# Kernel tuning notes

Measured on AMD Instinct MI355X. Metric: run time of the kernel, lower is better.

## Reference

```python
import jax, jax.numpy as jnp
import numpy as np

B, S, D, H, NS = 4, 2048, 1024, 16, 300
DK = D // H                      # 64
NSP = (NS + H - 1) // H * H      # 304 (padded skills)
DG = NSP // H                    # 19
NEG_FILL = -1e9                  # fp32 path in the torch module


def setup_inputs() -> dict:
    key = jax.random.key(0)
    ks = jax.random.split(key, 12)
    sc = 0.02
    return {
        "context_sequence": jax.random.normal(ks[0], (B, S, D), jnp.float32),
        "value_sequence": jax.random.normal(ks[1], (B, S, NS), jnp.float32),
        "mask": jnp.triu(jnp.ones((S, S), jnp.bool_), k=1),  # causal: True = masked
        # weights stored as [in, out] (math-equivalent to torch's x @ W.T + b)
        "Wq": jax.random.normal(ks[2], (D, D), jnp.float32) * sc,
        "bq": jnp.zeros((D,), jnp.float32),
        "Wk": jax.random.normal(ks[3], (D, D), jnp.float32) * sc,
        "bk": jnp.zeros((D,), jnp.float32),
        "Wv": jax.random.normal(ks[4], (NS, NS), jnp.float32) * sc,
        "bv": jnp.zeros((NS,), jnp.float32),
        "Wg": jax.random.normal(ks[5], (NS, D), jnp.float32) * sc,  # gain_to_context
        "bg": jnp.zeros((D,), jnp.float32),
        "Wo": jax.random.normal(ks[6], (D, D), jnp.float32) * sc,   # output_proj
        "bo": jnp.zeros((D,), jnp.float32),
    }


def reference(context_sequence, value_sequence, mask,
              Wq, bq, Wk, bk, Wv, bv, Wg, bg, Wo, bo):
    b = context_sequence.shape[0]
    orig_dtype = context_sequence.dtype

    # Q, K: [b, H, S, DK]
    Q = (context_sequence @ Wq + bq).reshape(b, -1, H, DK).transpose(0, 2, 1, 3)
    K = (context_sequence @ Wk + bk).reshape(b, -1, H, DK).transpose(0, 2, 1, 3)

    # intrinsic-gain V: project in skill space, zero-pad to NSP, split heads -> [b, H, S, DG]
    V_proj = value_sequence @ Wv + bv
    V_proj = jnp.pad(V_proj, ((0, 0), (0, 0), (0, NSP - NS)))
    V = V_proj.reshape(b, -1, H, DG).transpose(0, 2, 1, 3)

    # fp32 score upcast, scale by sqrt(d_k), mask, cast back, softmax
    scores = jnp.einsum('bhqd,bhkd->bhqk',
                        Q.astype(jnp.float32), K.astype(jnp.float32)) / np.sqrt(DK)
    scores = jnp.where(mask, NEG_FILL, scores).astype(orig_dtype)
    attn = jax.nn.softmax(scores, axis=-1)

    # [b, H, S, DG] -> [b, S, NSP] -> slice to NS
    head_gains = jnp.einsum('bhqk,bhkd->bhqd', attn, V)
    agg = head_gains.transpose(0, 2, 1, 3).reshape(b, -1, NSP)[..., :NS]

    output = agg @ Wg + bg            # gain_to_context
    return output @ Wo + bo           # output_proj (dropout is identity in eval)
```

## Files before the change

### kernel.cpp

```cpp
#include <hip/hip_runtime.h>
#include <hip/hip_bf16.h>

#define MROWS 8192
#define DMODEL 1024
#define SLEN 2048
#define NHEADS 16
#define DKH 64
#define DGH 19
#define NSKILL 300
#define KGPAD 320
#define AGG_LD 320
#define QK_LD 2048
#define VK 320
#define VTN 384

typedef __attribute__((ext_vector_type(8))) short short8;
typedef __attribute__((ext_vector_type(4))) float floatx4;

__device__ __forceinline__ float bf2f(unsigned short u) {
  union { unsigned int i; float f; } cv;
  cv.i = ((unsigned int)u) << 16;
  return cv.f;
}
__device__ __forceinline__ unsigned short f2bf(float f) {
  __hip_bfloat16 h = __float2bfloat16(f);
  unsigned short u;
  __builtin_memcpy(&u, &h, 2);
  return u;
}

__device__ __forceinline__ void ld8(const float* p, float* v) {
  float4 a = *(const float4*)p;
  float4 b = *((const float4*)p + 1);
  v[0]=a.x; v[1]=a.y; v[2]=a.z; v[3]=a.w;
  v[4]=b.x; v[5]=b.y; v[6]=b.z; v[7]=b.w;
}
__device__ __forceinline__ void st1(float* p, float v) { *p = v; }
__device__ __forceinline__ void st1(__hip_bfloat16* p, float v) {
  unsigned short raw = f2bf(v); __builtin_memcpy(p, &raw, 2);
}
__device__ __forceinline__ void st8(__hip_bfloat16* p, const float* v) {
  ushort4 a, b;
  a.x=f2bf(v[0]); a.y=f2bf(v[1]); a.z=f2bf(v[2]); a.w=f2bf(v[3]);
  b.x=f2bf(v[4]); b.y=f2bf(v[5]); b.z=f2bf(v[6]); b.w=f2bf(v[7]);
  *(ushort4*)p = a;
  *((ushort4*)p + 1) = b;
}

__device__ __forceinline__ void gl_lds16(const void* g, void* l) {
  __builtin_amdgcn_global_load_lds(
      (const __attribute__((address_space(1))) unsigned int*)g,
      (__attribute__((address_space(3))) unsigned int*)l, 16, 0, 0);
}

__global__ __launch_bounds__(256)
void convert_bf16_kernel(const float* __restrict__ in,
                         __hip_bfloat16* __restrict__ out, int nelem)
{
  int i = (blockIdx.x * 256 + threadIdx.x) * 4;
  if (i < nelem) {
    float4 v = *(const float4*)(in + i);
    ushort4 s;
    s.x = f2bf(v.x); s.y = f2bf(v.y); s.z = f2bf(v.z); s.w = f2bf(v.w);
    *(ushort4*)((__hip_bfloat16*)out + i) = s;
  }
}

__global__ __launch_bounds__(256)
void convert_v_kernel(const float* __restrict__ in,
                      __hip_bfloat16* __restrict__ out)
{
  int idx = blockIdx.x * 256 + threadIdx.x;
  int row = idx / 40;
  int c8  = (idx - row * 40) * 8;
  const float* ip = in + (size_t)row * NSKILL + c8;
  float v[8];
  if (c8 + 8 <= NSKILL) {
    ld8(ip, v);
  } else {
    #pragma unroll
    for (int u = 0; u < 8; u++)
      v[u] = (c8 + u < NSKILL) ? ip[u] : 0.f;
  }
  st8(out + (size_t)row * VK + c8, v);
}

__global__ __launch_bounds__(256)
void convert_wg_kernel(const float* __restrict__ Wg,
                       __hip_bfloat16* __restrict__ Wgb)
{
  int i4 = (blockIdx.x * 256 + threadIdx.x) * 4;
  int r = i4 >> 10;
  ushort4 s = {0, 0, 0, 0};
  if (r < NSKILL) {
    float4 v = *(const float4*)(Wg + i4);
    s.x = f2bf(v.x); s.y = f2bf(v.y); s.z = f2bf(v.z); s.w = f2bf(v.w);
  }
  *(ushort4*)((__hip_bfloat16*)Wgb + i4) = s;
}

__global__ __launch_bounds__(256)
void build_biases_kernel(const float* __restrict__ bq, const float* __restrict__ bk,
                         const float* __restrict__ bv,
                         float* __restrict__ biasqk, float* __restrict__ biasv,
                         float* __restrict__ z384)
{
  int t = threadIdx.x;
  for (int i = t; i < 1024; i += 256) { biasqk[i] = bq[i]; biasqk[1024 + i] = bk[i]; }
  for (int i = t; i < 384; i += 256) {
    biasv[i] = (i < NSKILL) ? bv[i] : 0.f;
    z384[i] = 0.f;
  }
}

__global__ __launch_bounds__(256)
void bgo_kernel(const float* __restrict__ bg, const float* __restrict__ Wo,
                const float* __restrict__ bo, float* __restrict__ bgo)
{
  __shared__ float red[256];
  const int c   = threadIdx.x & 15;
  const int jg  = threadIdx.x >> 4;
  const int col = blockIdx.x * 16 + c;
  float acc = 0.f;
  const int j0 = jg * 64;
  #pragma unroll 8
  for (int j = j0; j < j0 + 64; j++)
    acc = fmaf(bg[j], Wo[(size_t)j * DMODEL + col], acc);
  red[threadIdx.x] = acc;
  __syncthreads();
  if (jg == 0) {
    float s = 0.f;
    #pragma unroll
    for (int g = 0; g < 16; g++) s += red[g*16 + c];
    bgo[col] = s + bo[col];
  }
}

__global__ __launch_bounds__(256)
void transpose_w_kernel(const float* __restrict__ W,
                        __hip_bfloat16* __restrict__ Wt,
                        int K, int Nld, int Ntrue, int Kpad)
{
  __shared__ float t[32][33];
  const int k0 = blockIdx.x * 32;
  const int n0 = blockIdx.y * 32;
  const int tx = threadIdx.x & 31, ty = threadIdx.x >> 5;
  #pragma unroll
  for (int i = 0; i < 4; i++) {
    int k = k0 + ty + i*8;
    int nn = n0 + tx;
    t[ty + i*8][tx] = (k < K && nn < Ntrue) ? W[(size_t)k * Nld + nn] : 0.f;
  }
  __syncthreads();
  #pragma unroll
  for (int i = 0; i < 4; i++) {
    int nn = n0 + ty + i*8;
    int kk = k0 + tx;
    st1(Wt + (size_t)nn * Kpad + kk, t[tx][ty + i*8]);
  }
}

template<typename TC>
__global__ __launch_bounds__(256)
void gemm_mfma_bt(const __hip_bfloat16* __restrict__ A,
                  const __hip_bfloat16* __restrict__ Bt,
                  const float* __restrict__ bias,
                  TC* __restrict__ C, int ldc,
                  int M, int N, int K, int lda, int ldb)
{
  __shared__ __align__(16) short Al[128*64];
  __shared__ __align__(16) short Bl[128*64];
  const int tid  = threadIdx.x;
  const int lane = tid & 63;
  const int wave = tid >> 6;
  const int wy = wave >> 1;
  const int wx = wave & 1;
  const int n    = lane & 15;
  const int quad = lane >> 4;

  const int m0 = blockIdx.y * 128;
  const int n0 = blockIdx.x * 128;

  floatx4 acc[4][4];
  #pragma unroll
  for (int i = 0; i < 4; i++)
    #pragma unroll
    for (int j = 0; j < 4; j++) acc[i][j] = (floatx4){0.f,0.f,0.f,0.f};

  const short* Ag = (const short*)A;
  const short* Bg = (const short*)Bt;

  for (int k0 = 0; k0 < K; k0 += 64) {
    #pragma unroll
    for (int it = 0; it < 4; it++) {
      int ci = it*256 + tid;
      int r = ci >> 3, c = ci & 7;
      int cs = c ^ (r & 7);
      gl_lds16(Ag + (size_t)(m0 + r) * lda + k0 + cs*8, &Al[ci*8]);
    }
    #pragma unroll
    for (int it = 0; it < 4; it++) {
      int ci = it*256 + tid;
      int r = ci >> 3, c = ci & 7;
      int cs = c ^ (r & 7);
      gl_lds16(Bg + (size_t)(n0 + r) * ldb + k0 + cs*8, &Bl[ci*8]);
    }
    __syncthreads();

    #pragma unroll
    for (int s = 0; s < 2; s++) {
      short8 af[4], bfr[4];
      const int c = s*4 + quad;
      #pragma unroll
      for (int i = 0; i < 4; i++) {
        int r = wy*64 + i*16 + n;
        af[i] = *(const short8*)&Al[(r*8 + (c ^ (r & 7)))*8];
      }
      #pragma unroll
      for (int j = 0; j < 4; j++) {
        int r = wx*64 + j*16 + n;
        bfr[j] = *(const short8*)&Bl[(r*8 + (c ^ (r & 7)))*8];
      }
      #pragma unroll
      for (int i = 0; i < 4; i++)
        #pragma unroll
        for (int j = 0; j < 4; j++)
          acc[i][j] = __builtin_amdgcn_mfma_f32_16x16x32_bf16(af[i], bfr[j], acc[i][j], 0, 0, 0);
    }
    __syncthreads();
  }

  float bj[4];
  #pragma unroll
  for (int j = 0; j < 4; j++) bj[j] = bias[n0 + wx*64 + j*16 + n];
  #pragma unroll
  for (int i = 0; i < 4; i++) {
    #pragma unroll
    for (int r = 0; r < 4; r++) {
      int row = m0 + wy*64 + i*16 + quad*4 + r;
      TC* cp = C + (size_t)row * ldc;
      #pragma unroll
      for (int j = 0; j < 4; j++) {
        int col = n0 + wx*64 + j*16 + n;
        st1(cp + col, acc[i][j][r] + bj[j]);
      }
    }
  }
}

__global__ __launch_bounds__(256)
void gemm_mfma_bt_tv(const __hip_bfloat16* __restrict__ A,
                     const __hip_bfloat16* __restrict__ Bt,
                     const float* __restrict__ bias,
                     __hip_bfloat16* __restrict__ VT,
                     int M, int N, int K, int lda, int ldb)
{
  __shared__ __align__(16) short Al[128*64];
  __shared__ __align__(16) short Bl[128*64];
  const int tid  = threadIdx.x;
  const int lane = tid & 63;
  const int wave = tid >> 6;
  const int wy = wave >> 1;
  const int wx = wave & 1;
  const int n    = lane & 15;
  const int quad = lane >> 4;

  const int m0 = blockIdx.y * 128;
  const int n0 = blockIdx.x * 128;

  floatx4 acc[4][4];
  #pragma unroll
  for (int i = 0; i < 4; i++)
    #pragma unroll
    for (int j = 0; j < 4; j++) acc[i][j] = (floatx4){0.f,0.f,0.f,0.f};

  const short* Ag = (const short*)A;
  const short* Bg = (const short*)Bt;

  for (int k0 = 0; k0 < K; k0 += 64) {
    #pragma unroll
    for (int it = 0; it < 4; it++) {
      int ci = it*256 + tid;
      int r = ci >> 3, c = ci & 7;
      int cs = c ^ (r & 7);
      gl_lds16(Ag + (size_t)(m0 + r) * lda + k0 + cs*8, &Al[ci*8]);
    }
    #pragma unroll
    for (int it = 0; it < 4; it++) {
      int ci = it*256 + tid;
      int r = ci >> 3, c = ci & 7;
      int cs = c ^ (r & 7);
      gl_lds16(Bg + (size_t)(n0 + r) * ldb + k0 + cs*8, &Bl[ci*8]);
    }
    __syncthreads();

    #pragma unroll
    for (int s = 0; s < 2; s++) {
      short8 af[4], bfr[4];
      const int c = s*4 + quad;
      #pragma unroll
      for (int i = 0; i < 4; i++) {
        int r = wy*64 + i*16 + n;
        af[i] = *(const short8*)&Al[(r*8 + (c ^ (r & 7)))*8];
      }
      #pragma unroll
      for (int j = 0; j < 4; j++) {
        int r = wx*64 + j*16 + n;
        bfr[j] = *(const short8*)&Bl[(r*8 + (c ^ (r & 7)))*8];
      }
      #pragma unroll
      for (int i = 0; i < 4; i++)
        #pragma unroll
        for (int j = 0; j < 4; j++)
          acc[i][j] = __builtin_amdgcn_mfma_f32_16x16x32_bf16(af[i], bfr[j], acc[i][j], 0, 0, 0);
    }
    __syncthreads();
  }

  float bj[4];
  #pragma unroll
  for (int j = 0; j < 4; j++) bj[j] = bias[n0 + wx*64 + j*16 + n];
  #pragma unroll
  for (int i = 0; i < 4; i++) {
    int row0 = m0 + wy*64 + i*16 + quad*4;
    int bb = row0 >> 11, rin = row0 & 2047;
    #pragma unroll
    for (int j = 0; j < 4; j++) {
      int col = n0 + wx*64 + j*16 + n;
      ushort4 pk;
      pk.x = f2bf(acc[i][j][0] + bj[j]);
      pk.y = f2bf(acc[i][j][1] + bj[j]);
      pk.z = f2bf(acc[i][j][2] + bj[j]);
      pk.w = f2bf(acc[i][j][3] + bj[j]);
      *(ushort4*)(VT + ((size_t)bb * VTN + col) * SLEN + rin) = pk;
    }
  }
}

#define ATT_BM 128
#define ATT_BK 64
#define ATT_GRID 1024

__global__ __launch_bounds__(256)
void attn_mfma_kernel(const __hip_bfloat16* __restrict__ Qb,
                      const __hip_bfloat16* __restrict__ Kb,
                      const __hip_bfloat16* __restrict__ VTg,
                      __hip_bfloat16* __restrict__ Agg)
{
  __shared__ __align__(16) short Kf[64*64];
  __shared__ __align__(16) short Vf[32*64];
  __shared__ __align__(16) unsigned int Pl[4][2][2][4][16][4];

  const int tid  = threadIdx.x;
  const int lane = tid & 63;
  const int wave = tid >> 6;
  const int n    = lane & 15;
  const int quad = lane >> 4;

  const int raw = blockIdx.x;
  const int grp = raw >> 6;
  const int qt  = (grp < 8) ? (15 - grp) : (grp - 8);
  const int bh  = raw & 63;
  const int h   = bh & 15;
  const int b   = bh >> 4;
  const int qbase = qt * ATT_BM;
  const size_t bS = (size_t)b * SLEN;

  short8 qf[2][2];
  #pragma unroll
  for (int rf = 0; rf < 2; rf++)
    #pragma unroll
    for (int ks = 0; ks < 2; ks++) {
      const __hip_bfloat16* qp = Qb + (bS + qbase + wave*32 + rf*16 + n) * QK_LD
                                    + h*DKH + ks*32 + quad*8;
      short8 v = *(const short8*)qp;
      #pragma unroll
      for (int e = 0; e < 8; e++) {
        float f = bf2f((unsigned short)v[e]) * 0.125f;
        v[e] = (short)f2bf(f);
      }
      qf[rf][ks] = v;
    }

  const short* kp;
  {
    int f = tid;
    int nn = f & 15, q = (f >> 4) & 3, c = (f >> 6) & 3;
    kp = (const short*)Kb + (bS + c*16 + nn) * QK_LD + h*DKH + q*8;
  }
  const short* vp;
  {
    int g = tid;
    int vn = g & 15, vq = (g >> 4) & 3, sv = (g >> 6) & 1, cv = g >> 7;
    vp = (const short*)VTg + ((size_t)b * VTN + h*DGH + cv*16 + vn) * SLEN
         + sv*32 + vq*8;
  }

  floatx4 of[2][2];
  float mrow[2], lrow[2];
  #pragma unroll
  for (int rf = 0; rf < 2; rf++) {
    #pragma unroll
    for (int cv = 0; cv < 2; cv++) of[rf][cv] = (floatx4){0.f,0.f,0.f,0.f};
    mrow[rf] = -1e30f; lrow[rf] = 0.f;
  }

  const int ntiles = (qbase + ATT_BM + ATT_BK - 1) / ATT_BK;
  const int wrow_max = qbase + wave*32 + 31;

  for (int kt = 0; kt < ntiles; kt++) {
    const int kbase = kt * ATT_BK;

    gl_lds16(kp,      &Kf[tid*8]);
    gl_lds16(kp + 32, &Kf[(tid + 256)*8]);
    gl_lds16(vp,      &Vf[tid*8]);
    kp += 64 * QK_LD;
    vp += 64;
    __syncthreads();

    if (kbase <= wrow_max) {
      short8 kfr[4][2];
      #pragma unroll
      for (int cf = 0; cf < 4; cf++)
        #pragma unroll
        for (int s = 0; s < 2; s++)
          kfr[cf][s] = *(const short8*)&Kf[((s*4 + cf)*64 + lane)*8];

      floatx4 sf[2][4];
      __builtin_amdgcn_s_setprio(1);
      #pragma unroll
      for (int rf = 0; rf < 2; rf++)
        #pragma unroll
        for (int cf = 0; cf < 4; cf++) {
          floatx4 a2 = (floatx4){0.f,0.f,0.f,0.f};
          a2 = __builtin_amdgcn_mfma_f32_16x16x32_bf16(kfr[cf][0], qf[rf][0], a2, 0, 0, 0);
          a2 = __builtin_amdgcn_mfma_f32_16x16x32_bf16(kfr[cf][1], qf[rf][1], a2, 0, 0, 0);
          sf[rf][cf] = a2;
        }
      __builtin_amdgcn_s_setprio(0);

      #pragma unroll
      for (int rf = 0; rf < 2; rf++) {
        const int qrow = qbase + wave*32 + rf*16 + n;
        if (kbase + 63 > qbase + wave*32 + rf*16) {
          #pragma unroll
          for (int cf = 0; cf < 4; cf++)
            #pragma unroll
            for (int r = 0; r < 4; r++) {
              int key = kbase + cf*16 + quad*4 + r;
              if (key > qrow) sf[rf][cf][r] = -INFINITY;
            }
        }
        float m0 = sf[rf][0][0];
        #pragma unroll
        for (int cf = 0; cf < 4; cf++)
          #pragma unroll
          for (int r = 0; r < 4; r++) m0 = fmaxf(m0, sf[rf][cf][r]);
        m0 = fmaxf(m0, __shfl_xor(m0, 16));
        m0 = fmaxf(m0, __shfl_xor(m0, 32));
        float mnew = fmaxf(mrow[rf], m0);
        float alpha = __expf(mrow[rf] - mnew);
        mrow[rf] = mnew;
        float rs = 0.f;
        #pragma unroll
        for (int cf = 0; cf < 4; cf++)
          #pragma unroll
          for (int r = 0; r < 4; r++) {
            float p = __expf(sf[rf][cf][r] - mnew);
            sf[rf][cf][r] = p;
            rs += p;
          }
        rs += __shfl_xor(rs, 16);
        rs += __shfl_xor(rs, 32);
        lrow[rf] = lrow[rf] * alpha + rs;
        #pragma unroll
        for (int cv = 0; cv < 2; cv++)
          #pragma unroll
          for (int r = 0; r < 4; r++) of[rf][cv][r] *= alpha;

        #pragma unroll
        for (int cf = 0; cf < 4; cf++) {
          unsigned int w0 = (unsigned int)f2bf(sf[rf][cf][0])
                          | ((unsigned int)f2bf(sf[rf][cf][1]) << 16);
          unsigned int w1 = (unsigned int)f2bf(sf[rf][cf][2])
                          | ((unsigned int)f2bf(sf[rf][cf][3]) << 16);
          int s   = cf >> 1;
          int qt2 = 2*(cf & 1) + (quad >> 1);
          int jp  = 2*(quad & 1);
          *(uint2*)&Pl[wave][rf][s][qt2][n][jp] = make_uint2(w0, w1);
        }
      }

      short8 vfr[2][2];
      #pragma unroll
      for (int cv = 0; cv < 2; cv++)
        #pragma unroll
        for (int s = 0; s < 2; s++)
          vfr[cv][s] = *(const short8*)&Vf[((cv*2 + s)*64 + lane)*8];

      __builtin_amdgcn_s_setprio(1);
      #pragma unroll
      for (int rf = 0; rf < 2; rf++) {
        short8 p0 = *(const short8*)&Pl[wave][rf][0][quad][n][0];
        short8 p1 = *(const short8*)&Pl[wave][rf][1][quad][n][0];
        #pragma unroll
        for (int cv = 0; cv < 2; cv++) {
          floatx4 a2 = of[rf][cv];
          a2 = __builtin_amdgcn_mfma_f32_16x16x32_bf16(vfr[cv][0], p0, a2, 0, 0, 0);
          a2 = __builtin_amdgcn_mfma_f32_16x16x32_bf16(vfr[cv][1], p1, a2, 0, 0, 0);
          of[rf][cv] = a2;
        }
      }
      __builtin_amdgcn_s_setprio(0);
    }
    __syncthreads();
  }

  #pragma unroll
  for (int rf = 0; rf < 2; rf++) {
    float inv = 1.f / lrow[rf];
    int row = qbase + wave*32 + rf*16 + n;
    __hip_bfloat16* op = Agg + (bS + row)*AGG_LD + h*DGH;
    #pragma unroll
    for (int cv = 0; cv < 2; cv++)
      #pragma unroll
      for (int r = 0; r < 4; r++) {
        int dim = cv*16 + quad*4 + r;
        if (dim < DGH) st1(op + dim, of[rf][cv][r] * inv);
      }
  }

  if (h == 15) {
    int row = qbase + (tid >> 1);
    int c0 = 304 + (tid & 1) * 8;
    float z[8] = {0.f,0.f,0.f,0.f,0.f,0.f,0.f,0.f};
    st8(Agg + (bS + row)*AGG_LD + c0, z);
  }
}

extern "C" void kernel_launch(void* const* d_in, const int* in_sizes, int n_in,
                              void* d_out, int out_size, void* d_ws, size_t ws_size,
                              hipStream_t stream) {
  const float* X   = (const float*)d_in[0];
  const float* Vin = (const float*)d_in[1];
  const float* Wq  = (const float*)d_in[3];
  const float* bq  = (const float*)d_in[4];
  const float* Wk  = (const float*)d_in[5];
  const float* bk  = (const float*)d_in[6];
  const float* Wv  = (const float*)d_in[7];
  const float* bv  = (const float*)d_in[8];
  const float* Wg  = (const float*)d_in[9];
  const float* bg  = (const float*)d_in[10];
  const float* Wo  = (const float*)d_in[11];
  const float* bo  = (const float*)d_in[12];
  float* out = (float*)d_out;

  char* ws = (char*)d_ws;
  __hip_bfloat16* Xb    = (__hip_bfloat16*)(ws);
  __hip_bfloat16* VT    = (__hip_bfloat16*)(ws);
  __hip_bfloat16* AggB  = (__hip_bfloat16*)(ws + 6291456);
  __hip_bfloat16* Wgb   = (__hip_bfloat16*)(ws + 11796480);
  __hip_bfloat16* WgoT  = (__hip_bfloat16*)(ws + 12582912);
  float*          bgoW  = (float*)         (ws + 13369344);
  __hip_bfloat16* WoT   = (__hip_bfloat16*)(ws + 13631488);
  __hip_bfloat16* QKbuf = (__hip_bfloat16*)(ws + 16777216);
  __hip_bfloat16* Wvt   = (__hip_bfloat16*)(ws + 50331648);

  char* ob = (char*)d_out;
  __hip_bfloat16* Wtqk   = (__hip_bfloat16*)(ob);
  float*          biasqk = (float*)(ob + 4194304);
  __hip_bfloat16* Vb16   = (__hip_bfloat16*)(ob + 4202496);
  float*          biasv  = (float*)(ob + 9445376);
  float*          z384   = (float*)(ob + 9446912);

  dim3 blk(256);
  convert_bf16_kernel<<<dim3(8192), blk, 0, stream>>>(X, Xb, MROWS*DMODEL);
  convert_v_kernel<<<dim3(1280), blk, 0, stream>>>(Vin, Vb16);
  transpose_w_kernel<<<dim3(32, 32), blk, 0, stream>>>(Wq, Wtqk, DMODEL, DMODEL, DMODEL, DMODEL);
  transpose_w_kernel<<<dim3(32, 32), blk, 0, stream>>>(Wk, Wtqk + 1024*1024, DMODEL, DMODEL, DMODEL, DMODEL);
  transpose_w_kernel<<<dim3(10, 12), blk, 0, stream>>>(Wv, Wvt, NSKILL, NSKILL, NSKILL, VK);
  build_biases_kernel<<<dim3(1), blk, 0, stream>>>(bq, bk, bv, biasqk, biasv, z384);

  gemm_mfma_bt<__hip_bfloat16><<<dim3(16, 64), blk, 0, stream>>>(
      Xb, Wtqk, biasqk, QKbuf, QK_LD, MROWS, QK_LD, DMODEL, DMODEL, DMODEL);

  transpose_w_kernel<<<dim3(32, 32), blk, 0, stream>>>(Wo, WoT, DMODEL, DMODEL, DMODEL, DMODEL);
  convert_wg_kernel<<<dim3(384), blk, 0, stream>>>(Wg, Wgb);
  gemm_mfma_bt<__hip_bfloat16><<<dim3(3, 8), blk, 0, stream>>>(
      WoT, Wgb, z384, WgoT, 384, DMODEL, 384, DMODEL, DMODEL, DMODEL);
  bgo_kernel<<<dim3(64), blk, 0, stream>>>(bg, Wo, bo, bgoW);

  gemm_mfma_bt_tv<<<dim3(3, 64), blk, 0, stream>>>(
      Vb16, Wvt, biasv, VT, MROWS, VTN, VK, VK, VK);

  attn_mfma_kernel<<<dim3(ATT_GRID), dim3(256), 0, stream>>>(
      QKbuf, QKbuf + 1024, VT, AggB);

  gemm_mfma_bt<float><<<dim3(8, 64), blk, 0, stream>>>(
      AggB, WgoT, bgoW, out, DMODEL, MROWS, DMODEL, KGPAD, KGPAD, 384);
}
```

Measured before the change: 324.1 us.

## Double-buffer K/V tiles in attention and merge prep kernels

The attention kernel now uses two LDS buffers for K and V tiles, issuing the next tile's global-to-LDS loads before computing on the current one, with explicit vmcnt waits and barriers. This replaces the load-then-sync-then-compute loop so memory latency can overlap with MFMA work. Separately, the conversion, bias and weight-transpose kernels are fused into two launches, and some buffers are relocated to cut launch overhead. The change doubles attention LDS use, which may reduce occupancy, and assumes an even number of key tiles.

```diff
diff --git a/kernel.cpp b/kernel.cpp
--- a/kernel.cpp
+++ b/kernel.cpp
@@ -54,62 +54,54 @@
 }
 
 __global__ __launch_bounds__(256)
-void convert_bf16_kernel(const float* __restrict__ in,
-                         __hip_bfloat16* __restrict__ out, int nelem)
-{
-  int i = (blockIdx.x * 256 + threadIdx.x) * 4;
-  if (i < nelem) {
-    float4 v = *(const float4*)(in + i);
-    ushort4 s;
-    s.x = f2bf(v.x); s.y = f2bf(v.y); s.z = f2bf(v.z); s.w = f2bf(v.w);
-    *(ushort4*)((__hip_bfloat16*)out + i) = s;
-  }
-}
-
-__global__ __launch_bounds__(256)
-void convert_v_kernel(const float* __restrict__ in,
-                      __hip_bfloat16* __restrict__ out)
-{
-  int idx = blockIdx.x * 256 + threadIdx.x;
-  int row = idx / 40;
-  int c8  = (idx - row * 40) * 8;
-  const float* ip = in + (size_t)row * NSKILL + c8;
-  float v[8];
-  if (c8 + 8 <= NSKILL) {
-    ld8(ip, v);
-  } else {
-    #pragma unroll
-    for (int u = 0; u < 8; u++)
-      v[u] = (c8 + u < NSKILL) ? ip[u] : 0.f;
-  }
-  st8(out + (size_t)row * VK + c8, v);
-}
-
-__global__ __launch_bounds__(256)
-void convert_wg_kernel(const float* __restrict__ Wg,
-                       __hip_bfloat16* __restrict__ Wgb)
-{
-  int i4 = (blockIdx.x * 256 + threadIdx.x) * 4;
-  int r = i4 >> 10;
-  ushort4 s = {0, 0, 0, 0};
-  if (r < NSKILL) {
-    float4 v = *(const float4*)(Wg + i4);
-    s.x = f2bf(v.x); s.y = f2bf(v.y); s.z = f2bf(v.z); s.w = f2bf(v.w);
-  }
-  *(ushort4*)((__hip_bfloat16*)Wgb + i4) = s;
-}
-
-__global__ __launch_bounds__(256)
-void build_biases_kernel(const float* __restrict__ bq, const float* __restrict__ bk,
+void prep_convert_kernel(const float* __restrict__ X,
+                         const float* __restrict__ Vin,
+                         const float* __restrict__ Wg,
+                         const float* __restrict__ bq, const float* __restrict__ bk,
                          const float* __restrict__ bv,
+                         __hip_bfloat16* __restrict__ Xb,
+                         __hip_bfloat16* __restrict__ Vb16,
+                         __hip_bfloat16* __restrict__ Wgb,
                          float* __restrict__ biasqk, float* __restrict__ biasv,
                          float* __restrict__ z384)
 {
-  int t = threadIdx.x;
-  for (int i = t; i < 1024; i += 256) { biasqk[i] = bq[i]; biasqk[1024 + i] = bk[i]; }
-  for (int i = t; i < 384; i += 256) {
-    biasv[i] = (i < NSKILL) ? bv[i] : 0.f;
-    z384[i] = 0.f;
+  const int bid = blockIdx.x;
+  const int t = threadIdx.x;
+  if (bid < 8192) {
+    int i = (bid * 256 + t) * 4;
+    float4 v = *(const float4*)(X + i);
+    ushort4 s;
+    s.x = f2bf(v.x); s.y = f2bf(v.y); s.z = f2bf(v.z); s.w = f2bf(v.w);
+    *(ushort4*)((__hip_bfloat16*)Xb + i) = s;
+  } else if (bid < 9472) {
+    int idx = (bid - 8192) * 256 + t;
+    int row = idx / 40;
+    int c8  = (idx - row * 40) * 8;
+    const float* ip = Vin + (size_t)row * NSKILL + c8;
+    float v[8];
+    if (c8 + 8 <= NSKILL) {
+      ld8(ip, v);
+    } else {
+      #pragma unroll
+      for (int u = 0; u < 8; u++)
+        v[u] = (c8 + u < NSKILL) ? ip[u] : 0.f;
+    }
+    st8(Vb16 + (size_t)row * VK + c8, v);
+  } else if (bid < 9856) {
+    int i4 = ((bid - 9472) * 256 + t) * 4;
+    int r = i4 >> 10;
+    ushort4 s = {0, 0, 0, 0};
+    if (r < NSKILL) {
+      float4 v = *(const float4*)(Wg + i4);
+      s.x = f2bf(v.x); s.y = f2bf(v.y); s.z = f2bf(v.z); s.w = f2bf(v.w);
+    }
+    *(ushort4*)((__hip_bfloat16*)Wgb + i4) = s;
+  } else {
+    for (int i = t; i < 1024; i += 256) { biasqk[i] = bq[i]; biasqk[1024 + i] = bk[i]; }
+    for (int i = t; i < 384; i += 256) {
+      biasv[i] = (i < NSKILL) ? bv[i] : 0.f;
+      z384[i] = 0.f;
+    }
   }
 }
 
@@ -137,10 +129,21 @@
 }
 
 __global__ __launch_bounds__(256)
-void transpose_w_kernel(const float* __restrict__ W,
-                        __hip_bfloat16* __restrict__ Wt,
-                        int K, int Nld, int Ntrue, int Kpad)
+void transpose_all_kernel(const float* __restrict__ Wq, const float* __restrict__ Wk,
+                          const float* __restrict__ Wo, const float* __restrict__ Wv,
+                          __hip_bfloat16* __restrict__ Wtqk,
+                          __hip_bfloat16* __restrict__ WoT,
+                          __hip_bfloat16* __restrict__ Wvt)
 {
+  const int z = blockIdx.z;
+  const float* W; __hip_bfloat16* Wt; int K, Nld, Ntrue, Kpad;
+  if (z == 0)      { W = Wq; Wt = Wtqk;             K=1024; Nld=1024; Ntrue=1024; Kpad=1024; }
+  else if (z == 1) { W = Wk; Wt = Wtqk + 1024*1024; K=1024; Nld=1024; Ntrue=1024; Kpad=1024; }
+  else if (z == 2) { W = Wo; Wt = WoT;              K=1024; Nld=1024; Ntrue=1024; Kpad=1024; }
+  else {
+    if (blockIdx.x >= 10 || blockIdx.y >= 12) return;
+    W = Wv; Wt = Wvt; K=NSKILL; Nld=NSKILL; Ntrue=NSKILL; Kpad=VK;
+  }
   __shared__ float t[32][33];
   const int k0 = blockIdx.x * 32;
   const int n0 = blockIdx.y * 32;
@@ -347,8 +350,8 @@
                       const __hip_bfloat16* __restrict__ VTg,
                       __hip_bfloat16* __restrict__ Agg)
 {
-  __shared__ __align__(16) short Kf[64*64];
-  __shared__ __align__(16) short Vf[32*64];
+  __shared__ __align__(16) short Kf[2][64*64];
+  __shared__ __align__(16) short Vf[2][32*64];
   __shared__ __align__(16) unsigned int Pl[4][2][2][4][16][4];
 
   const int tid  = threadIdx.x;
@@ -405,115 +408,135 @@
     mrow[rf] = -1e30f; lrow[rf] = 0.f;
   }
 
-  const int ntiles = (qbase + ATT_BM + ATT_BK - 1) / ATT_BK;
+  const int ntiles = (qbase + ATT_BM) / ATT_BK;
   const int wrow_max = qbase + wave*32 + 31;
 
-  for (int kt = 0; kt < ntiles; kt++) {
-    const int kbase = kt * ATT_BK;
-
-    gl_lds16(kp,      &Kf[tid*8]);
-    gl_lds16(kp + 32, &Kf[(tid + 256)*8]);
-    gl_lds16(vp,      &Vf[tid*8]);
+  auto stage = [&](int buf) {
+    gl_lds16(kp,      &Kf[buf][tid*8]);
+    gl_lds16(kp + 32, &Kf[buf][(tid + 256)*8]);
+    gl_lds16(vp,      &Vf[buf][tid*8]);
     kp += 64 * QK_LD;
     vp += 64;
-    __syncthreads();
-
-    if (kbase <= wrow_max) {
-      short8 kfr[4][2];
-      #pragma unroll
-      for (int cf = 0; cf < 4; cf++)
-        #pragma unroll
-        for (int s = 0; s < 2; s++)
-          kfr[cf][s] = *(const short8*)&Kf[((s*4 + cf)*64 + lane)*8];
-
-      floatx4 sf[2][4];
-      __builtin_amdgcn_s_setprio(1);
-      #pragma unroll
-      for (int rf = 0; rf < 2; rf++)
-        #pragma unroll
-        for (int cf = 0; cf < 4; cf++) {
-          floatx4 a2 = (floatx4){0.f,0.f,0.f,0.f};
-          a2 = __builtin_amdgcn_mfma_f32_16x16x32_bf16(kfr[cf][0], qf[rf][0], a2, 0, 0, 0);
-          a2 = __builtin_amdgcn_mfma_f32_16x16x32_bf16(kfr[cf][1], qf[rf][1], a2, 0, 0, 0);
-          sf[rf][cf] = a2;
-        }
-      __builtin_amdgcn_s_setprio(0);
-
-      #pragma unroll
-      for (int rf = 0; rf < 2; rf++) {
-        const int qrow = qbase + wave*32 + rf*16 + n;
-        if (kbase + 63 > qbase + wave*32 + rf*16) {
-          #pragma unroll
-          for (int cf = 0; cf < 4; cf++)
-            #pragma unroll
-            for (int r = 0; r < 4; r++) {
-              int key = kbase + cf*16 + quad*4 + r;
-              if (key > qrow) sf[rf][cf][r] = -INFINITY;
-            }
-        }
-        float m0 = sf[rf][0][0];
-        #pragma unroll
-        for (int cf = 0; cf < 4; cf++)
-          #pragma unroll
-          for (int r = 0; r < 4; r++) m0 = fmaxf(m0, sf[rf][cf][r]);
-        m0 = fmaxf(m0, __shfl_xor(m0, 16));
-        m0 = fmaxf(m0, __shfl_xor(m0, 32));
-        float mnew = fmaxf(mrow[rf], m0);
-        float alpha = __expf(mrow[rf] - mnew);
-        mrow[rf] = mnew;
-        float rs = 0.f;
+  };
+
+  auto compute_tile = [&](int buf, int kbase) {
+    if (kbase > wrow_max) return;
+    short8 kfr[4][2];
+    #pragma unroll
+    for (int cf = 0; cf < 4; cf++)
+      #pragma unroll
+      for (int s = 0; s < 2; s++)
+        kfr[cf][s] = *(const short8*)&Kf[buf][((s*4 + cf)*64 + lane)*8];
+
+    floatx4 sf[2][4];
+    __builtin_amdgcn_s_setprio(1);
+    #pragma unroll
+    for (int rf = 0; rf < 2; rf++)
+      #pragma unroll
+      for (int cf = 0; cf < 4; cf++) {
+        floatx4 a2 = (floatx4){0.f,0.f,0.f,0.f};
+        a2 = __builtin_amdgcn_mfma_f32_16x16x32_bf16(kfr[cf][0], qf[rf][0], a2, 0, 0, 0);
+        a2 = __builtin_amdgcn_mfma_f32_16x16x32_bf16(kfr[cf][1], qf[rf][1], a2, 0, 0, 0);
+        sf[rf][cf] = a2;
+      }
+    __builtin_amdgcn_s_setprio(0);
+
+    #pragma unroll
+    for (int rf = 0; rf < 2; rf++) {
+      const int qrow = qbase + wave*32 + rf*16 + n;
+      if (kbase + 63 > qbase + wave*32 + rf*16) {
         #pragma unroll
         for (int cf = 0; cf < 4; cf++)
           #pragma unroll
           for (int r = 0; r < 4; r++) {
-            float p = __expf(sf[rf][cf][r] - mnew);
-            sf[rf][cf][r] = p;
-            rs += p;
+            int key = kbase + cf*16 + quad*4 + r;
+            if (key > qrow) sf[rf][cf][r] = -INFINITY;
           }
-        rs += __shfl_xor(rs, 16);
-        rs += __shfl_xor(rs, 32);
-        lrow[rf] = lrow[rf] * alpha + rs;
+      }
+      float m0 = sf[rf][0][0];
+      #pragma unroll
+      for (int cf = 0; cf < 4; cf++)
         #pragma unroll
-        for (int cv = 0; cv < 2; cv++)
-          #pragma unroll
-          for (int r = 0; r < 4; r++) of[rf][cv][r] *= alpha;
-
+        for (int r = 0; r < 4; r++) m0 = fmaxf(m0, sf[rf][cf][r]);
+      m0 = fmaxf(m0, __shfl_xor(m0, 16));
+      m0 = fmaxf(m0, __shfl_xor(m0, 32));
+      float mnew = fmaxf(mrow[rf], m0);
+      float alpha = __expf(mrow[rf] - mnew);
+      mrow[rf] = mnew;
+      float rs = 0.f;
+      #pragma unroll
+      for (int cf = 0; cf < 4; cf++)
         #pragma unroll
-        for (int cf = 0; cf < 4; cf++) {
-          unsigned int w0 = (unsigned int)f2bf(sf[rf][cf][0])
-                          | ((unsigned int)f2bf(sf[rf][cf][1]) << 16);
-          unsigned int w1 = (unsigned int)f2bf(sf[rf][cf][2])
-                          | ((unsigned int)f2bf(sf[rf][cf][3]) << 16);
-          int s   = cf >> 1;
-          int qt2 = 2*(cf & 1) + (quad >> 1);
-          int jp  = 2*(quad & 1);
-          *(uint2*)&Pl[wave][rf][s][qt2][n][jp] = make_uint2(w0, w1);
+        for (int r = 0; r < 4; r++) {
+          float p = __expf(sf[rf][cf][r] - mnew);
+          sf[rf][cf][r] = p;
+          rs += p;
         }
-      }
-
-      short8 vfr[2][2];
+      rs += __shfl_xor(rs, 16);
+      rs += __shfl_xor(rs, 32);
+      lrow[rf] = lrow[rf] * alpha + rs;
       #pragma unroll
       for (int cv = 0; cv < 2; cv++)
         #pragma unroll
-        for (int s = 0; s < 2; s++)
-          vfr[cv][s] = *(const short8*)&Vf[((cv*2 + s)*64 + lane)*8];
-
-      __builtin_amdgcn_s_setprio(1);
-      #pragma unroll
-      for (int rf = 0; rf < 2; rf++) {
-        short8 p0 = *(const short8*)&Pl[wave][rf][0][quad][n][0];
-        short8 p1 = *(const short8*)&Pl[wave][rf][1][quad][n][0];
-        #pragma unroll
-        for (int cv = 0; cv < 2; cv++) {
-          floatx4 a2 = of[rf][cv];
-          a2 = __builtin_amdgcn_mfma_f32_16x16x32_bf16(vfr[cv][0], p0, a2, 0, 0, 0);
-          a2 = __builtin_amdgcn_mfma_f32_16x16x32_bf16(vfr[cv][1], p1, a2, 0, 0, 0);
-          of[rf][cv] = a2;
-        }
-      }
-      __builtin_amdgcn_s_setprio(0);
-    }
-    __syncthreads();
+        for (int r = 0; r < 4; r++) of[rf][cv][r] *= alpha;
+
+      #pragma unroll
+      for (int cf = 0; cf < 4; cf++) {
+        unsigned int w0 = (unsigned int)f2bf(sf[rf][cf][0])
+                        | ((unsigned int)f2bf(sf[rf][cf][1]) << 16);
+        unsigned int w1 = (unsigned int)f2bf(sf[rf][cf][2])
+                        | ((unsigned int)f2bf(sf[rf][cf][3]) << 16);
+        int s   = cf >> 1;
+        int qt2 = 2*(cf & 1) + (quad >> 1);
+        int jp  = 2*(quad & 1);
+        *(uint2*)&Pl[wave][rf][s][qt2][n][jp] = make_uint2(w0, w1);
+      }
+    }
+
+    short8 vfr[2][2];
+    #pragma unroll
+    for (int cv = 0; cv < 2; cv++)
+      #pragma unroll
+      for (int s = 0; s < 2; s++)
+        vfr[cv][s] = *(const short8*)&Vf[buf][((cv*2 + s)*64 + lane)*8];
+
+    __builtin_amdgcn_s_setprio(1);
+    #pragma unroll
+    for (int rf = 0; rf < 2; rf++) {
+      short8 p0 = *(const short8*)&Pl[wave][rf][0][quad][n][0];
+      short8 p1 = *(const short8*)&Pl[wave][rf][1][quad][n][0];
+      #pragma unroll
+      for (int cv = 0; cv < 2; cv++) {
+        floatx4 a2 = of[rf][cv];
+        a2 = __builtin_amdgcn_mfma_f32_16x16x32_bf16(vfr[cv][0], p0, a2, 0, 0, 0);
+        a2 = __builtin_amdgcn_mfma_f32_16x16x32_bf16(vfr[cv][1], p1, a2, 0, 0, 0);
+        of[rf][cv] = a2;
+      }
+    }
+    __builtin_amdgcn_s_setprio(0);
+  };
+
+  stage(0);
+  for (int kt = 0; kt < ntiles; kt += 2) {
+    stage(1);
+    asm volatile("s_waitcnt vmcnt(3)" ::: "memory");
+    __builtin_amdgcn_s_barrier();
+    __builtin_amdgcn_sched_barrier(0);
+    compute_tile(0, kt * ATT_BK);
+    __builtin_amdgcn_sched_barrier(0);
+    __builtin_amdgcn_s_barrier();
+
+    if (kt + 2 < ntiles) {
+      stage(0);
+      asm volatile("s_waitcnt vmcnt(3)" ::: "memory");
+    } else {
+      asm volatile("s_waitcnt vmcnt(0)" ::: "memory");
+    }
+    __builtin_amdgcn_s_barrier();
+    __builtin_amdgcn_sched_barrier(0);
+    compute_tile(1, (kt + 1) * ATT_BK);
+    __builtin_amdgcn_sched_barrier(0);
+    __builtin_amdgcn_s_barrier();
   }
 
   #pragma unroll
@@ -559,12 +582,10 @@
   __hip_bfloat16* Xb    = (__hip_bfloat16*)(ws);
   __hip_bfloat16* VT    = (__hip_bfloat16*)(ws);
   __hip_bfloat16* AggB  = (__hip_bfloat16*)(ws + 6291456);
-  __hip_bfloat16* Wgb   = (__hip_bfloat16*)(ws + 11796480);
   __hip_bfloat16* WgoT  = (__hip_bfloat16*)(ws + 12582912);
   float*          bgoW  = (float*)         (ws + 13369344);
-  __hip_bfloat16* WoT   = (__hip_bfloat16*)(ws + 13631488);
   __hip_bfloat16* QKbuf = (__hip_bfloat16*)(ws + 16777216);
-  __hip_bfloat16* Wvt   = (__hip_bfloat16*)(ws + 50331648);
+  __hip_bfloat16* WoT   = (__hip_bfloat16*)(ws + 50331648);
 
   char* ob = (char*)d_out;
   __hip_bfloat16* Wtqk   = (__hip_bfloat16*)(ob);
@@ -572,23 +593,21 @@
   __hip_bfloat16* Vb16   = (__hip_bfloat16*)(ob + 4202496);
   float*          biasv  = (float*)(ob + 9445376);
   float*          z384   = (float*)(ob + 9446912);
+  __hip_bfloat16* Wgb    = (__hip_bfloat16*)(ob + 9448448);
+  __hip_bfloat16* Wvt    = (__hip_bfloat16*)(ob + 10234880);
 
   dim3 blk(256);
-  convert_bf16_kernel<<<dim3(8192), blk, 0, stream>>>(X, Xb, MROWS*DMODEL);
-  convert_v_kernel<<<dim3(1280), blk, 0, stream>>>(Vin, Vb16);
-  transpose_w_kernel<<<dim3(32, 32), blk, 0, stream>>>(Wq, Wtqk, DMODEL, DMODEL, DMODEL, DMODEL);
-  transpose_w_kernel<<<dim3(32, 32), blk, 0, stream>>>(Wk, Wtqk + 1024*1024, DMODEL, DMODEL, DMODEL, DMODEL);
-  transpose_w_kernel<<<dim3(10, 12), blk, 0, stream>>>(Wv, Wvt, NSKILL, NSKILL, NSKILL, VK);
-  build_biases_kernel<<<dim3(1), blk, 0, stream>>>(bq, bk, bv, biasqk, biasv, z384);
+  prep_convert_kernel<<<dim3(9857), blk, 0, stream>>>(
+      X, Vin, Wg, bq, bk, bv, Xb, Vb16, Wgb, biasqk, biasv, z384);
+  transpose_all_kernel<<<dim3(32, 32, 4), blk, 0, stream>>>(
+      Wq, Wk, Wo, Wv, Wtqk, WoT, Wvt);
 
   gemm_mfma_bt<__hip_bfloat16><<<dim3(16, 64), blk, 0, stream>>>(
       Xb, Wtqk, biasqk, QKbuf, QK_LD, MROWS, QK_LD, DMODEL, DMODEL, DMODEL);
 
-  transpose_w_kernel<<<dim3(32, 32), blk, 0, stream>>>(Wo, WoT, DMODEL, DMODEL, DMODEL, DMODEL);
-  convert_wg_kernel<<<dim3(384), blk, 0, stream>>>(Wg, Wgb);
+  bgo_kernel<<<dim3(64), blk, 0, stream>>>(bg, Wo, bo, bgoW);
   gemm_mfma_bt<__hip_bfloat16><<<dim3(3, 8), blk, 0, stream>>>(
       WoT, Wgb, z384, WgoT, 384, DMODEL, 384, DMODEL, DMODEL, DMODEL);
-  bgo_kernel<<<dim3(64), blk, 0, stream>>>(bg, Wo, bo, bgoW);
 
   gemm_mfma_bt_tv<<<dim3(3, 64), blk, 0, stream>>>(
       Vb16, Wvt, biasv, VT, MROWS, VTN, VK, VK, VK);
```

New measurement: 297.4 us. 8.2% less time.
